# Performance work log

Measured on AMD Instinct MI355X. Metric: run time of the kernel, lower is better.

Reference implementation:

```python
import jax, jax.numpy as jnp
import numpy as np
from jax import lax

T, B, D, H = 1024, 64, 512, 512


def _elman_layer(x_seq, Wih, bih, Whh, bhh):
    """x_seq: [T, B, in]; returns hidden sequence [T, B, out].
    Input-side GEMM is precomputed across all timesteps; the recurrence
    (h @ Whh^T + bhh, tanh) runs in a lax.scan with state resident.
    """
    xs = jnp.einsum('tbi,hi->tbh', x_seq, Wih) + bih  # [T, B, H]
    h0 = jnp.zeros((x_seq.shape[1], Whh.shape[0]), dtype=x_seq.dtype)

    def step(h, xt):
        h_new = jnp.tanh(xt + h @ Whh.T + bhh)
        return h_new, h_new

    _, ys = lax.scan(step, h0, xs)
    return ys


def setup_inputs() -> dict:
    key = jax.random.key(0)
    ks = jax.random.split(key, 9)
    stdv = 1.0 / np.sqrt(H)
    u = lambda k, shape: jax.random.uniform(k, shape, jnp.float32, -stdv, stdv)
    return {
        'Xt': jax.random.normal(ks[0], (T, B, D), jnp.float32),
        'ihW0': u(ks[1], (H, D)),
        'ihB0': u(ks[2], (H,)),
        'hhW0': u(ks[3], (H, H)),
        'hhB0': u(ks[4], (H,)),
        'ihW1': u(ks[5], (H, H)),
        'ihB1': u(ks[6], (H,)),
        'hhW1': u(ks[7], (H, H)),
        'hhB1': u(ks[8], (H,)),
    }


def reference(Xt, ihW0, ihB0, hhW0, hhB0, ihW1, ihB1, hhW1, hhB1):
    # 2-layer Elman RNN, tanh activation, zero initial hidden state,
    # dropout=0 (eval), stack_output=True -> output [T, B, H].
    y0 = _elman_layer(Xt, ihW0, ihB0, hhW0, hhB0)
    y1 = _elman_layer(y0, ihW1, ihB1, hhW1, hhB1)
    return y1
```

## Files before the change

kernel.cpp:

```cpp
#include <hip/hip_runtime.h>
#include <math.h>
#include <stdint.h>

#define TT      1024
#define BATCH   64
#define HH      512
#define NG      8
#define WPG     32
#define BSL     8
#define HSL     16
#define NTH     512
#define SP      516
#define WLDS    (4 * 16 * SP)
#define STG_FL  (8 * 256)
#define LDS_FL  (WLDS + 3 * STG_FL)
#define LDS_BYTES (LDS_FL * 4)

__device__ __forceinline__ float2 sys_ld2(const float* p) {
    unsigned long long v = __hip_atomic_load((const unsigned long long*)p, __ATOMIC_RELAXED,
                                             __HIP_MEMORY_SCOPE_SYSTEM);
    union { unsigned long long u; float2 f; } cv; cv.u = v; return cv.f;
}
__device__ __forceinline__ void sys_st(float* p, float v) {
    __hip_atomic_store(p, v, __ATOMIC_RELAXED, __HIP_MEMORY_SCOPE_SYSTEM);
}
__device__ __forceinline__ void wait_vm0() {
    asm volatile("s_waitcnt vmcnt(0)" ::: "memory");
}

__global__ void __launch_bounds__(NTH, 2)
elman_persistent(const float* __restrict__ Xt,
                 const float* __restrict__ Wih0, const float* __restrict__ bih0,
                 const float* __restrict__ Whh0, const float* __restrict__ bhh0,
                 const float* __restrict__ Wih1, const float* __restrict__ bih1,
                 const float* __restrict__ Whh1, const float* __restrict__ bhh1,
                 float* __restrict__ out,
                 float* h0buf,
                 unsigned* cnt)
{
    extern __shared__ float lds[];
    const int tid = threadIdx.x;
    const int g   = blockIdx.x & 7;
    const int w   = blockIdx.x >> 3;
    const int jg0 = w * HSL;
    const int bg0 = g * BSL;

    float* Wl  = lds;
    float* stg = lds + WLDS;

    for (int m = 0; m < 4; ++m) {
        const float* src = (m == 0) ? Wih0 : (m == 1) ? Whh0 : (m == 2) ? Wih1 : Whh1;
        for (int f = tid; f < 16 * 128; f += NTH) {
            int jj = f >> 7, k4 = f & 127;
            float4 v = ((const float4*)(src + (size_t)(jg0 + jj) * HH))[k4];
            *(float4*)(Wl + (m * 16 + jj) * SP + k4 * 4) = v;
        }
    }
    float bias = 0.f;
    if (tid < 256) {
        int layer = tid >> 7, jj = tid & 15;
        bias = layer ? (bih1[jg0 + jj] + bhh1[jg0 + jj])
                     : (bih0[jg0 + jj] + bhh0[jg0 + jj]);
    }
    __syncthreads();

    const int j      = tid & 15;
    const int ks     = tid >> 4;
    const int koff_t = ks * 8;
    const int b_st = tid >> 6;
    const int k_st = (tid & 63) * 4;

    unsigned* mycnt = cnt + g * 64;
    unsigned target = 0;

    float acc0[8], acc1[8];

    for (int p = 0; p <= TT; ++p) {
        const bool doL0  = (p < TT);
        const bool doL1  = (p >= 1);
        const bool hasH1 = (p >= 2);

        float4 xc0 = make_float4(0.f,0.f,0.f,0.f), xc1 = xc0;
        float2 h0a0, h0a1, h0b0, h0b1;
        float2 h1a0 = {0.f,0.f}, h1a1 = h1a0, h1b0 = h1a0, h1b1 = h1a0;
        if (doL0) {
            const float* xs = Xt + ((size_t)p * BATCH + bg0 + b_st) * HH + k_st;
            xc0 = *(const float4*)(xs);
            xc1 = *(const float4*)(xs + 256);
        }
        {
            const float* hs = h0buf + (size_t)((p + 1) & 1) * (BATCH * HH)
                            + (size_t)(bg0 + b_st) * HH + k_st;
            h0a0 = sys_ld2(hs);       h0a1 = sys_ld2(hs + 2);
            h0b0 = sys_ld2(hs + 256); h0b1 = sys_ld2(hs + 258);
        }
        if (hasH1) {
            const float* hs = out + ((size_t)(p - 2) * BATCH + bg0 + b_st) * HH + k_st;
            h1a0 = sys_ld2(hs);       h1a1 = sys_ld2(hs + 2);
            h1b0 = sys_ld2(hs + 256); h1b1 = sys_ld2(hs + 258);
        }

        #pragma unroll
        for (int b = 0; b < 8; ++b) { acc0[b] = 0.f; acc1[b] = 0.f; }

        auto st4 = [&](int s, float4 v) {
            *(float4*)(stg + (s % 3) * STG_FL + b_st * 256 + k_st) = v;
        };
        auto compute_x = [&](int c) {
            const float* wr  = Wl + (0 * 16 + j) * SP + c * 256 + koff_t;
            const float* sb  = stg + (c % 3) * STG_FL;
            #pragma unroll
            for (int u = 0; u < 2; ++u) {
                float4 wv = *(const float4*)(wr + u * 4);
                #pragma unroll
                for (int b = 0; b < 8; ++b) {
                    float4 xv = *(const float4*)(sb + b * 256 + koff_t + u * 4);
                    acc0[b] = fmaf(wv.x, xv.x, acc0[b]);
                    acc0[b] = fmaf(wv.y, xv.y, acc0[b]);
                    acc0[b] = fmaf(wv.z, xv.z, acc0[b]);
                    acc0[b] = fmaf(wv.w, xv.w, acc0[b]);
                }
            }
        };
        auto compute_h0 = [&](int c, int buf) {
            const float* w0 = Wl + (1 * 16 + j) * SP + c * 256 + koff_t;
            const float* w1 = Wl + (2 * 16 + j) * SP + c * 256 + koff_t;
            const float* sb = stg + buf * STG_FL;
            #pragma unroll
            for (int u = 0; u < 2; ++u) {
                float4 wa = *(const float4*)(w0 + u * 4);
                float4 wb = *(const float4*)(w1 + u * 4);
                #pragma unroll
                for (int b = 0; b < 8; ++b) {
                    float4 xv = *(const float4*)(sb + b * 256 + koff_t + u * 4);
                    if (doL0) {
                        acc0[b] = fmaf(wa.x, xv.x, acc0[b]);
                        acc0[b] = fmaf(wa.y, xv.y, acc0[b]);
                        acc0[b] = fmaf(wa.z, xv.z, acc0[b]);
                        acc0[b] = fmaf(wa.w, xv.w, acc0[b]);
                    }
                    if (doL1) {
                        acc1[b] = fmaf(wb.x, xv.x, acc1[b]);
                        acc1[b] = fmaf(wb.y, xv.y, acc1[b]);
                        acc1[b] = fmaf(wb.z, xv.z, acc1[b]);
                        acc1[b] = fmaf(wb.w, xv.w, acc1[b]);
                    }
                }
            }
        };
        auto compute_h1 = [&](int c, int buf) {
            const float* wr = Wl + (3 * 16 + j) * SP + c * 256 + koff_t;
            const float* sb = stg + buf * STG_FL;
            #pragma unroll
            for (int u = 0; u < 2; ++u) {
                float4 wv = *(const float4*)(wr + u * 4);
                #pragma unroll
                for (int b = 0; b < 8; ++b) {
                    float4 xv = *(const float4*)(sb + b * 256 + koff_t + u * 4);
                    acc1[b] = fmaf(wv.x, xv.x, acc1[b]);
                    acc1[b] = fmaf(wv.y, xv.y, acc1[b]);
                    acc1[b] = fmaf(wv.z, xv.z, acc1[b]);
                    acc1[b] = fmaf(wv.w, xv.w, acc1[b]);
                }
            }
        };

        if (doL0) st4(0, xc0);
        __syncthreads();
        if (doL0) { st4(1, xc1); compute_x(0); }
        __syncthreads();
        st4(2, make_float4(h0a0.x, h0a0.y, h0a1.x, h0a1.y));
        if (doL0) compute_x(1);
        __syncthreads();
        st4(3, make_float4(h0b0.x, h0b0.y, h0b1.x, h0b1.y));
        compute_h0(0, 2);
        __syncthreads();
        if (hasH1) st4(4, make_float4(h1a0.x, h1a0.y, h1a1.x, h1a1.y));
        compute_h0(1, 0);
        __syncthreads();
        if (hasH1) { st4(5, make_float4(h1b0.x, h1b0.y, h1b1.x, h1b1.y));
                     compute_h1(0, 1); }
        __syncthreads();
        if (hasH1) compute_h1(1, 2);

        #pragma unroll
        for (int b = 0; b < 8; ++b) {
            acc0[b] += __shfl_xor(acc0[b], 16);
            acc0[b] += __shfl_xor(acc0[b], 32);
            acc1[b] += __shfl_xor(acc1[b], 16);
            acc1[b] += __shfl_xor(acc1[b], 32);
        }
        const int lane = tid & 63;
        const int wv   = tid >> 6;
        if (lane < 16) {
            #pragma unroll
            for (int b = 0; b < 8; ++b) {
                stg[((wv * 2 + 0) * 8 + b) * 16 + lane] = acc0[b];
                stg[((wv * 2 + 1) * 8 + b) * 16 + lane] = acc1[b];
            }
        }
        __syncthreads();
        if (tid < 256) {
            const int layer = tid >> 7, b = (tid >> 4) & 7, jj = tid & 15;
            float s = 0.f;
            #pragma unroll
            for (int wq = 0; wq < 8; ++wq) s += stg[((wq * 2 + layer) * 8 + b) * 16 + jj];
            float val = tanhf(s + bias);
            if (layer == 0) {
                if (doL0) sys_st(h0buf + (size_t)(p & 1) * (BATCH * HH)
                                 + (size_t)(bg0 + b) * HH + jg0 + jj, val);
            } else {
                if (doL1) sys_st(out + ((size_t)(p - 1) * BATCH + bg0 + b) * HH + jg0 + jj, val);
            }
        }
        wait_vm0();
        __syncthreads();

        if (tid == 0) {
            __hip_atomic_fetch_add(mycnt, 1u, __ATOMIC_RELAXED, __HIP_MEMORY_SCOPE_SYSTEM);
            target += WPG;
            while (__hip_atomic_load(mycnt, __ATOMIC_RELAXED, __HIP_MEMORY_SCOPE_SYSTEM) < target)
                __builtin_amdgcn_s_sleep(2);
            asm volatile("" ::: "memory");
        } else {
            target += WPG;
        }
        __syncthreads();
    }
}

extern "C" void kernel_launch(void* const* d_in, const int* in_sizes, int n_in,
                              void* d_out, int out_size, void* d_ws, size_t ws_size,
                              hipStream_t stream) {
    (void)in_sizes; (void)n_in; (void)out_size; (void)ws_size;
    const float* Xt   = (const float*)d_in[0];
    const float* Wih0 = (const float*)d_in[1];
    const float* bih0 = (const float*)d_in[2];
    const float* Whh0 = (const float*)d_in[3];
    const float* bhh0 = (const float*)d_in[4];
    const float* Wih1 = (const float*)d_in[5];
    const float* bih1 = (const float*)d_in[6];
    const float* Whh1 = (const float*)d_in[7];
    const float* bhh1 = (const float*)d_in[8];
    float*    out   = (float*)d_out;
    float*    h0buf = (float*)d_ws;
    unsigned* cnt   = (unsigned*)((char*)d_ws + 2 * BATCH * HH * 4);

    hipFuncSetAttribute((const void*)elman_persistent,
                        hipFuncAttributeMaxDynamicSharedMemorySize, LDS_BYTES);
    hipMemsetAsync(d_ws, 0, 2 * BATCH * HH * 4 + NG * 256, stream);

    elman_persistent<<<dim3(NG * WPG), dim3(NTH), LDS_BYTES, stream>>>(
        Xt, Wih0, bih0, Whh0, bhh0, Wih1, bih1, Whh1, bhh1, out, h0buf, cnt);
}
```

Before: 6.984 ms.

## Keep weights in registers, prefetch next x step, cut per-step barriers

Weight slices for all four matrices are now held in registers (32 float4 per thread) instead of LDS, and each thread computes a 2-output by 4-batch tile. The input x for the next timestep is prefetched into a double-buffered LDS slot during the current step, so the x contribution is computed before the hidden-state barrier. The chain of six staged syncthreads per step is replaced by one staging barrier. A spin-count timeout on the grid counter wait is also added, which can silently skip synchronization. Register pressure rises sharply at 2 blocks/CU launch bounds, risking spills.

After: 22.16 ms. 3.17x slower.

```diff
diff --git a/kernel.cpp b/kernel.cpp
--- a/kernel.cpp
+++ b/kernel.cpp
@@ -10,10 +10,15 @@
 #define BSL     8
 #define HSL     16
 #define NTH     512
-#define SP      516
-#define WLDS    (4 * 16 * SP)
-#define STG_FL  (8 * 256)
-#define LDS_FL  (WLDS + 3 * STG_FL)
+
+#define SP2     516
+#define BUFX0   0
+#define BUFX1   (8 * SP2)
+#define BUFH0_  (16 * SP2)
+#define BUFH1_  (24 * SP2)
+#define SCR     (32 * SP2)
+#define SCRS    17
+#define LDS_FL  (SCR + 129 * SCRS)
 #define LDS_BYTES (LDS_FL * 4)
 
 __device__ __forceinline__ float2 sys_ld2(const float* p) {
@@ -26,6 +31,10 @@
 }
 __device__ __forceinline__ void wait_vm0() {
     asm volatile("s_waitcnt vmcnt(0)" ::: "memory");
+}
+__device__ __forceinline__ void dot4(float4 w, float4 x, float& a) {
+    a = fmaf(w.x, x.x, a); a = fmaf(w.y, x.y, a);
+    a = fmaf(w.z, x.z, a); a = fmaf(w.w, x.w, a);
 }
 
 __global__ void __launch_bounds__(NTH, 2)
@@ -45,182 +54,184 @@
     const int jg0 = w * HSL;
     const int bg0 = g * BSL;
 
-    float* Wl  = lds;
-    float* stg = lds + WLDS;
-
-    for (int m = 0; m < 4; ++m) {
-        const float* src = (m == 0) ? Wih0 : (m == 1) ? Whh0 : (m == 2) ? Wih1 : Whh1;
-        for (int f = tid; f < 16 * 128; f += NTH) {
-            int jj = f >> 7, k4 = f & 127;
-            float4 v = ((const float4*)(src + (size_t)(jg0 + jj) * HH))[k4];
-            *(float4*)(Wl + (m * 16 + jj) * SP + k4 * 4) = v;
-        }
-    }
+    const int jp   = tid & 7;
+    const int bb4  = ((tid >> 3) & 1) * 4;
+    const int ks   = tid >> 4;
+    const int kb   = ks * 4;
+    const int lane = tid & 63;
+    const int wv   = tid >> 6;
+
+    const int row = tid >> 6;
+    const int kst = (tid & 63) * 4;
+
+    float4 wr[4][2][4];
+    {
+        const float* const Ws[4] = {Wih0, Whh0, Wih1, Whh1};
+        #pragma unroll
+        for (int m = 0; m < 4; ++m)
+            #pragma unroll
+            for (int jj = 0; jj < 2; ++jj) {
+                const float* src = Ws[m] + (size_t)(jg0 + jp * 2 + jj) * HH + kb;
+                #pragma unroll
+                for (int u = 0; u < 4; ++u)
+                    wr[m][jj][u] = *(const float4*)(src + u * 128);
+            }
+    }
+
     float bias = 0.f;
     if (tid < 256) {
-        int layer = tid >> 7, jj = tid & 15;
-        bias = layer ? (bih1[jg0 + jj] + bhh1[jg0 + jj])
-                     : (bih0[jg0 + jj] + bhh0[jg0 + jj]);
+        const int l = tid >> 7, jx = jg0 + (tid & 15);
+        bias = l ? (bih1[jx] + bhh1[jx]) : (bih0[jx] + bhh0[jx]);
+    }
+
+    {
+        const float* xs = Xt + (size_t)(bg0 + row) * HH + kst;
+        *(float4*)(lds + BUFX0 + row * SP2 + kst)       = *(const float4*)(xs);
+        *(float4*)(lds + BUFX0 + row * SP2 + kst + 256) = *(const float4*)(xs + 256);
     }
     __syncthreads();
 
-    const int j      = tid & 15;
-    const int ks     = tid >> 4;
-    const int koff_t = ks * 8;
-    const int b_st = tid >> 6;
-    const int k_st = (tid & 63) * 4;
+    const float* xload  = Xt  + ((size_t)BATCH + bg0 + row) * HH + kst;
+    const float* h1load = out + (size_t)(bg0 + row) * HH + kst;
 
     unsigned* mycnt = cnt + g * 64;
     unsigned target = 0;
-
-    float acc0[8], acc1[8];
+    bool     dead   = false;
 
     for (int p = 0; p <= TT; ++p) {
         const bool doL0  = (p < TT);
         const bool doL1  = (p >= 1);
         const bool hasH1 = (p >= 2);
-
-        float4 xc0 = make_float4(0.f,0.f,0.f,0.f), xc1 = xc0;
-        float2 h0a0, h0a1, h0b0, h0b1;
-        float2 h1a0 = {0.f,0.f}, h1a1 = h1a0, h1b0 = h1a0, h1b1 = h1a0;
-        if (doL0) {
-            const float* xs = Xt + ((size_t)p * BATCH + bg0 + b_st) * HH + k_st;
-            xc0 = *(const float4*)(xs);
-            xc1 = *(const float4*)(xs + 256);
-        }
+        const bool pre   = (p + 1 < TT);
+        const int  cur   = p & 1;
+
+        float2 h0a, h0b, h0c, h0d;
         {
             const float* hs = h0buf + (size_t)((p + 1) & 1) * (BATCH * HH)
-                            + (size_t)(bg0 + b_st) * HH + k_st;
-            h0a0 = sys_ld2(hs);       h0a1 = sys_ld2(hs + 2);
-            h0b0 = sys_ld2(hs + 256); h0b1 = sys_ld2(hs + 258);
-        }
+                            + (size_t)(bg0 + row) * HH + kst;
+            h0a = sys_ld2(hs);       h0b = sys_ld2(hs + 2);
+            h0c = sys_ld2(hs + 256); h0d = sys_ld2(hs + 258);
+        }
+        float2 h1a = {0.f, 0.f}, h1b = h1a, h1c = h1a, h1d = h1a;
         if (hasH1) {
-            const float* hs = out + ((size_t)(p - 2) * BATCH + bg0 + b_st) * HH + k_st;
-            h1a0 = sys_ld2(hs);       h1a1 = sys_ld2(hs + 2);
-            h1b0 = sys_ld2(hs + 256); h1b1 = sys_ld2(hs + 258);
-        }
-
+            h1a = sys_ld2(h1load);       h1b = sys_ld2(h1load + 2);
+            h1c = sys_ld2(h1load + 256); h1d = sys_ld2(h1load + 258);
+            h1load += BATCH * HH;
+        }
+        float4 xn0, xn1;
+        if (pre) { xn0 = *(const float4*)(xload); xn1 = *(const float4*)(xload + 256);
+                   xload += BATCH * HH; }
+
+        float acc0[2][4], acc1[2][4];
         #pragma unroll
-        for (int b = 0; b < 8; ++b) { acc0[b] = 0.f; acc1[b] = 0.f; }
-
-        auto st4 = [&](int s, float4 v) {
-            *(float4*)(stg + (s % 3) * STG_FL + b_st * 256 + k_st) = v;
+        for (int jj = 0; jj < 2; ++jj)
+            #pragma unroll
+            for (int bi = 0; bi < 4; ++bi) { acc0[jj][bi] = 0.f; acc1[jj][bi] = 0.f; }
+
+        if (doL0) {
+            const float* bx = lds + (cur ? BUFX1 : BUFX0);
+            #pragma unroll
+            for (int u = 0; u < 4; ++u)
+                #pragma unroll
+                for (int bi = 0; bi < 4; ++bi) {
+                    float4 xv = *(const float4*)(bx + (bb4 + bi) * SP2 + kb + u * 128);
+                    dot4(wr[0][0][u], xv, acc0[0][bi]);
+                    dot4(wr[0][1][u], xv, acc0[1][bi]);
+                }
+        }
+        __builtin_amdgcn_sched_barrier(0);
+
+        *(float4*)(lds + BUFH0_ + row * SP2 + kst)       = make_float4(h0a.x, h0a.y, h0b.x, h0b.y);
+        *(float4*)(lds + BUFH0_ + row * SP2 + kst + 256) = make_float4(h0c.x, h0c.y, h0d.x, h0d.y);
+        if (hasH1) {
+            *(float4*)(lds + BUFH1_ + row * SP2 + kst)       = make_float4(h1a.x, h1a.y, h1b.x, h1b.y);
+            *(float4*)(lds + BUFH1_ + row * SP2 + kst + 256) = make_float4(h1c.x, h1c.y, h1d.x, h1d.y);
+        }
+        __syncthreads();
+
+        auto h0pass = [&](bool d0, bool d1) {
+            #pragma unroll
+            for (int u = 0; u < 4; ++u)
+                #pragma unroll
+                for (int bi = 0; bi < 4; ++bi) {
+                    float4 hv = *(const float4*)(lds + BUFH0_ + (bb4 + bi) * SP2 + kb + u * 128);
+                    if (d0) { dot4(wr[1][0][u], hv, acc0[0][bi]);
+                              dot4(wr[1][1][u], hv, acc0[1][bi]); }
+                    if (d1) { dot4(wr[2][0][u], hv, acc1[0][bi]);
+                              dot4(wr[2][1][u], hv, acc1[1][bi]); }
+                }
         };
-        auto compute_x = [&](int c) {
-            const float* wr  = Wl + (0 * 16 + j) * SP + c * 256 + koff_t;
-            const float* sb  = stg + (c % 3) * STG_FL;
-            #pragma unroll
-            for (int u = 0; u < 2; ++u) {
-                float4 wv = *(const float4*)(wr + u * 4);
-                #pragma unroll
-                for (int b = 0; b < 8; ++b) {
-                    float4 xv = *(const float4*)(sb + b * 256 + koff_t + u * 4);
-                    acc0[b] = fmaf(wv.x, xv.x, acc0[b]);
-                    acc0[b] = fmaf(wv.y, xv.y, acc0[b]);
-                    acc0[b] = fmaf(wv.z, xv.z, acc0[b]);
-                    acc0[b] = fmaf(wv.w, xv.w, acc0[b]);
-                }
-            }
-        };
-        auto compute_h0 = [&](int c, int buf) {
-            const float* w0 = Wl + (1 * 16 + j) * SP + c * 256 + koff_t;
-            const float* w1 = Wl + (2 * 16 + j) * SP + c * 256 + koff_t;
-            const float* sb = stg + buf * STG_FL;
-            #pragma unroll
-            for (int u = 0; u < 2; ++u) {
-                float4 wa = *(const float4*)(w0 + u * 4);
-                float4 wb = *(const float4*)(w1 + u * 4);
-                #pragma unroll
-                for (int b = 0; b < 8; ++b) {
-                    float4 xv = *(const float4*)(sb + b * 256 + koff_t + u * 4);
-                    if (doL0) {
-                        acc0[b] = fmaf(wa.x, xv.x, acc0[b]);
-                        acc0[b] = fmaf(wa.y, xv.y, acc0[b]);
-                        acc0[b] = fmaf(wa.z, xv.z, acc0[b]);
-                        acc0[b] = fmaf(wa.w, xv.w, acc0[b]);
-                    }
-                    if (doL1) {
-                        acc1[b] = fmaf(wb.x, xv.x, acc1[b]);
-                        acc1[b] = fmaf(wb.y, xv.y, acc1[b]);
-                        acc1[b] = fmaf(wb.z, xv.z, acc1[b]);
-                        acc1[b] = fmaf(wb.w, xv.w, acc1[b]);
-                    }
-                }
-            }
-        };
-        auto compute_h1 = [&](int c, int buf) {
-            const float* wr = Wl + (3 * 16 + j) * SP + c * 256 + koff_t;
-            const float* sb = stg + buf * STG_FL;
-            #pragma unroll
-            for (int u = 0; u < 2; ++u) {
-                float4 wv = *(const float4*)(wr + u * 4);
-                #pragma unroll
-                for (int b = 0; b < 8; ++b) {
-                    float4 xv = *(const float4*)(sb + b * 256 + koff_t + u * 4);
-                    acc1[b] = fmaf(wv.x, xv.x, acc1[b]);
-                    acc1[b] = fmaf(wv.y, xv.y, acc1[b]);
-                    acc1[b] = fmaf(wv.z, xv.z, acc1[b]);
-                    acc1[b] = fmaf(wv.w, xv.w, acc1[b]);
-                }
-            }
-        };
-
-        if (doL0) st4(0, xc0);
-        __syncthreads();
-        if (doL0) { st4(1, xc1); compute_x(0); }
-        __syncthreads();
-        st4(2, make_float4(h0a0.x, h0a0.y, h0a1.x, h0a1.y));
-        if (doL0) compute_x(1);
-        __syncthreads();
-        st4(3, make_float4(h0b0.x, h0b0.y, h0b1.x, h0b1.y));
-        compute_h0(0, 2);
-        __syncthreads();
-        if (hasH1) st4(4, make_float4(h1a0.x, h1a0.y, h1a1.x, h1a1.y));
-        compute_h0(1, 0);
-        __syncthreads();
-        if (hasH1) { st4(5, make_float4(h1b0.x, h1b0.y, h1b1.x, h1b1.y));
-                     compute_h1(0, 1); }
-        __syncthreads();
-        if (hasH1) compute_h1(1, 2);
+        if (doL0 && doL1) h0pass(true, true);
+        else if (doL0)    h0pass(true, false);
+        else              h0pass(false, true);
+        if (hasH1) {
+            #pragma unroll
+            for (int u = 0; u < 4; ++u)
+                #pragma unroll
+                for (int bi = 0; bi < 4; ++bi) {
+                    float4 hv = *(const float4*)(lds + BUFH1_ + (bb4 + bi) * SP2 + kb + u * 128);
+                    dot4(wr[3][0][u], hv, acc1[0][bi]);
+                    dot4(wr[3][1][u], hv, acc1[1][bi]);
+                }
+        }
 
         #pragma unroll
-        for (int b = 0; b < 8; ++b) {
-            acc0[b] += __shfl_xor(acc0[b], 16);
-            acc0[b] += __shfl_xor(acc0[b], 32);
-            acc1[b] += __shfl_xor(acc1[b], 16);
-            acc1[b] += __shfl_xor(acc1[b], 32);
-        }
-        const int lane = tid & 63;
-        const int wv   = tid >> 6;
+        for (int jj = 0; jj < 2; ++jj)
+            #pragma unroll
+            for (int bi = 0; bi < 4; ++bi) {
+                acc0[jj][bi] += __shfl_xor(acc0[jj][bi], 16);
+                acc0[jj][bi] += __shfl_xor(acc0[jj][bi], 32);
+                acc1[jj][bi] += __shfl_xor(acc1[jj][bi], 16);
+                acc1[jj][bi] += __shfl_xor(acc1[jj][bi], 32);
+            }
         if (lane < 16) {
             #pragma unroll
-            for (int b = 0; b < 8; ++b) {
-                stg[((wv * 2 + 0) * 8 + b) * 16 + lane] = acc0[b];
-                stg[((wv * 2 + 1) * 8 + b) * 16 + lane] = acc1[b];
-            }
-        }
-        __syncthreads();
+            for (int jj = 0; jj < 2; ++jj)
+                #pragma unroll
+                for (int bi = 0; bi < 4; ++bi) {
+                    lds[SCR + (wv * 16 + jj * 4 + bi) * SCRS + lane]     = acc0[jj][bi];
+                    lds[SCR + (wv * 16 + 8 + jj * 4 + bi) * SCRS + lane] = acc1[jj][bi];
+                }
+        }
+        __syncthreads();
+
         if (tid < 256) {
-            const int layer = tid >> 7, b = (tid >> 4) & 7, jj = tid & 15;
+            const int l    = tid >> 7;
+            const int jloc = tid & 15;
+            const int blo  = (tid >> 4) & 7;
+            const int a    = l * 8 + (jloc & 1) * 4 + (blo & 3);
+            const int ll   = (jloc >> 1) + 8 * (blo >> 2);
             float s = 0.f;
             #pragma unroll
-            for (int wq = 0; wq < 8; ++wq) s += stg[((wq * 2 + layer) * 8 + b) * 16 + jj];
+            for (int wq = 0; wq < 8; ++wq)
+                s += lds[SCR + (wq * 16 + a) * SCRS + ll];
             float val = tanhf(s + bias);
-            if (layer == 0) {
-                if (doL0) sys_st(h0buf + (size_t)(p & 1) * (BATCH * HH)
-                                 + (size_t)(bg0 + b) * HH + jg0 + jj, val);
+            if (l == 0) {
+                if (doL0) sys_st(h0buf + (size_t)cur * (BATCH * HH)
+                                 + (size_t)(bg0 + blo) * HH + jg0 + jloc, val);
             } else {
-                if (doL1) sys_st(out + ((size_t)(p - 1) * BATCH + bg0 + b) * HH + jg0 + jj, val);
+                if (doL1) sys_st(out + ((size_t)(p - 1) * BATCH + bg0 + blo) * HH + jg0 + jloc, val);
             }
         }
         wait_vm0();
         __syncthreads();
+
+        if (pre) {
+            float* bx = lds + (cur ? BUFX0 : BUFX1);
+            *(float4*)(bx + row * SP2 + kst)       = xn0;
+            *(float4*)(bx + row * SP2 + kst + 256) = xn1;
+        }
 
         if (tid == 0) {
             __hip_atomic_fetch_add(mycnt, 1u, __ATOMIC_RELAXED, __HIP_MEMORY_SCOPE_SYSTEM);
             target += WPG;
-            while (__hip_atomic_load(mycnt, __ATOMIC_RELAXED, __HIP_MEMORY_SCOPE_SYSTEM) < target)
-                __builtin_amdgcn_s_sleep(2);
+            if (!dead) {
+                unsigned spins = 0;
+                while (__hip_atomic_load(mycnt, __ATOMIC_RELAXED, __HIP_MEMORY_SCOPE_SYSTEM) < target) {
+                    __builtin_amdgcn_s_sleep(2);
+                    if (++spins > (1u << 21)) { dead = true; break; }
+                }
+            }
             asm volatile("" ::: "memory");
         } else {
             target += WPG;
```
